# Optimization experiments

Hardware: AMD Instinct MI355X
Metric: run time of the kernel (lower is better)

## Reference

```python
import jax, jax.numpy as jnp
import numpy as np

P = 0.5          # dropout-style keep probability (wandb.config.probability)
Z = 1000         # number of Monte-Carlo normal draws in the original loop


def setup_inputs() -> dict:
    key = jax.random.key(0)
    k1, k2, k3 = jax.random.split(key, 3)
    B, D_in, H, C = 65536, 28 * 28, 256, 10
    x = jax.random.uniform(k1, (B, D_in), dtype=jnp.float32)          # pixel-like inputs in [0,1)
    W1 = jax.random.normal(k2, (H, D_in), dtype=jnp.float32) * 0.05   # fc1.weight
    W2 = jax.random.normal(k3, (C, H), dtype=jnp.float32) * 0.05      # fc2.weight
    return {"x": x, "W1": W1, "W2": W2}


def _mc_normal_layer(x, W, key):
    """Gaussian-dropout moment-propagation layer.

    Original torch code draws Z independent Normal(mean, std) samples and
    averages them, which is exactly Normal(mean, std / sqrt(Z)). We use the
    closed form: one eps draw instead of Z kernel launches.
    """
    mean = P * jnp.matmul(x, W.T)                                   # [B, out]
    var = P * (1.0 - P) * jnp.matmul(x * x, (W * W).T)              # [B, out]
    std = jnp.sqrt(var)
    eps = jax.random.normal(key, mean.shape, dtype=mean.dtype)
    return mean + std * (eps / jnp.sqrt(jnp.asarray(Z, mean.dtype)))


def reference(x, W1, W2):
    x = x.reshape(-1, 28 * 28)
    k1, k2 = jax.random.split(jax.random.key(42))
    h = jax.nn.relu(_mc_normal_layer(x, W1, k1))   # [B, H]
    out = _mc_normal_layer(h, W2, k2)              # [B, 10]
    return out
```

## Files before the change

### kernel.cpp

```cpp
#include <hip/hip_runtime.h>
#include <hip/hip_bf16.h>
#include <cstdint>


#define K_DIM 784
#define KP 800
#define N_HID 256
#define N_OUT 10
#define BM 64
#define NSTEP 25
#define WSQ_OFF (N_HID * KP)
#define W2_OFF (832 * 1024)
#define W2SQ 4096
#define H_OFF (1 << 20)
#define BM2 128

using short8 = __attribute__((ext_vector_type(8))) short;
using floatx4 = __attribute__((ext_vector_type(4))) float;
typedef uint16_t u16;

__host__ __device__ inline void threefry2x32(uint32_t k0, uint32_t k1,
                                             uint32_t x0, uint32_t x1,
                                             uint32_t& o0, uint32_t& o1) {
  uint32_t ks0 = k0, ks1 = k1, ks2 = k0 ^ k1 ^ 0x1BD11BDAu;
  x0 += ks0;
  x1 += ks1;
#define TFR(r) { x0 += x1; x1 = (x1 << (r)) | (x1 >> (32 - (r))); x1 ^= x0; }
  TFR(13) TFR(15) TFR(26) TFR(6)   x0 += ks1; x1 += ks2 + 1u;
  TFR(17) TFR(29) TFR(16) TFR(24)  x0 += ks2; x1 += ks0 + 2u;
  TFR(13) TFR(15) TFR(26) TFR(6)   x0 += ks0; x1 += ks1 + 3u;
  TFR(17) TFR(29) TFR(16) TFR(24)  x0 += ks1; x1 += ks2 + 4u;
  TFR(13) TFR(15) TFR(26) TFR(6)   x0 += ks2; x1 += ks0 + 5u;
#undef TFR
  o0 = x0;
  o1 = x1;
}

__device__ __forceinline__ float bits_to_normal(uint32_t bits) {
  const float lo = -0.99999994f;
  float u01 = __uint_as_float((bits >> 9) | 0x3F800000u) - 1.0f;
  float u = fmaxf(lo, u01 * 2.0f + lo);
  float w = -__logf((1.0f - u) * (1.0f + u));
  float p;
  if (w < 5.0f) {
    w -= 2.5f;
    p = 2.81022636e-08f;
    p = fmaf(p, w, 3.43273939e-07f);
    p = fmaf(p, w, -3.5233877e-06f);
    p = fmaf(p, w, -4.39150654e-06f);
    p = fmaf(p, w, 0.00021858087f);
    p = fmaf(p, w, -0.00125372503f);
    p = fmaf(p, w, -0.00417768164f);
    p = fmaf(p, w, 0.246640727f);
    p = fmaf(p, w, 1.50140941f);
  } else {
    w = sqrtf(w) - 3.0f;
    p = -0.000200214257f;
    p = fmaf(p, w, 0.000100950558f);
    p = fmaf(p, w, 0.00134934322f);
    p = fmaf(p, w, -0.00367342844f);
    p = fmaf(p, w, 0.00573950773f);
    p = fmaf(p, w, -0.0076224613f);
    p = fmaf(p, w, 0.00943887047f);
    p = fmaf(p, w, 1.00167406f);
    p = fmaf(p, w, 2.83297682f);
  }
  return 1.41421356f * (p * u);
}

__device__ __forceinline__ float eps_part(uint32_t ka, uint32_t kb, uint32_t i) {
  uint32_t o0, o1;
  threefry2x32(ka, kb, 0u, i, o0, o1);
  return bits_to_normal(o0 ^ o1);
}

__device__ __forceinline__ u16 cvt_bf16(float f) {
  union { __hip_bfloat16 h; u16 u; } c;
  c.h = __float2bfloat16(f);
  return c.u;
}

__device__ __forceinline__ float bf2f(u16 b) {
  return __uint_as_float((uint32_t)b << 16);
}

__global__ __launch_bounds__(256) void pack_w1(const float* __restrict__ W1,
                                               u16* __restrict__ bp) {
  const int col = blockIdx.x;
  for (int k = threadIdx.x; k < KP; k += 256) {
    float w = (k < K_DIM) ? W1[col * K_DIM + k] : 0.0f;
    bp[col * KP + k] = cvt_bf16(w);
    bp[WSQ_OFF + col * KP + k] = cvt_bf16(w * w);
  }
}

__global__ __launch_bounds__(256) void pack_w2(const float* __restrict__ W2,
                                               u16* __restrict__ w2p) {
#pragma unroll
  for (int i = 0; i < 16; ++i) {
    int g = threadIdx.x + i * 256;
    int col = g >> 8, k = g & 255;
    float w = (col < N_OUT) ? W2[col * N_HID + k] : 0.0f;
    w2p[g] = cvt_bf16(w);
    w2p[W2SQ + g] = cvt_bf16(w * w);
  }
}

__global__ __launch_bounds__(256, 4) void gemm1(
    const float* __restrict__ x, const u16* __restrict__ bp,
    u16* __restrict__ hws, uint32_t k1a, uint32_t k1b) {
  __shared__ u16 sA[2][2][BM * 32];

  const int tid = threadIdx.x;
  const int lane = tid & 63;
  const int l15 = lane & 15;
  const int lhal = lane >> 4;
  const int wn = tid >> 6;
  const int bid = blockIdx.x;
  const int gr0 = (bid >> 1) * BM;
  const int bc0 = (bid & 1) * 128;

  const int srow = tid >> 2;
  const int skq = (tid & 3) * 8;
  const float* xptr = x + (size_t)(gr0 + srow) * K_DIM + skq;
  const int sidx = (srow * 32 + skq) ^ ((srow & 7) << 3);

  const uint32_t boff0 = (uint32_t)(bc0 + wn * 32 + 0 * 16 + l15) * KP + (uint32_t)lhal * 8;
  const uint32_t boff1 = (uint32_t)(bc0 + wn * 32 + 1 * 16 + l15) * KP + (uint32_t)lhal * 8;

#define AIDX(i) ((((i * 16 + l15) * 32 + lhal * 8)) ^ (((i * 16 + l15) & 7) << 3))
  const int aidx0 = AIDX(0);
  const int aidx1 = AIDX(1);
  const int aidx2 = AIDX(2);
  const int aidx3 = AIDX(3);
#undef AIDX

#define DECL_ACC(i) \
  floatx4 am##i##0 = {0.f, 0.f, 0.f, 0.f}, am##i##1 = {0.f, 0.f, 0.f, 0.f}; \
  floatx4 av##i##0 = {0.f, 0.f, 0.f, 0.f}, av##i##1 = {0.f, 0.f, 0.f, 0.f};
  DECL_ACC(0) DECL_ACC(1) DECL_ACC(2) DECL_ACC(3)
#undef DECL_ACC

  float4 q0, q1;
  auto loadX = [&](int kk) {
    if (kk + skq + 8 <= K_DIM) {
      q0 = *reinterpret_cast<const float4*>(xptr + kk);
      q1 = *reinterpret_cast<const float4*>(xptr + kk + 4);
    } else {
      q0 = make_float4(0.f, 0.f, 0.f, 0.f);
      q1 = make_float4(0.f, 0.f, 0.f, 0.f);
    }
  };
  auto writeA = [&](int buf) {
    short8 va, v2;
    va[0] = (short)cvt_bf16(q0.x); v2[0] = (short)cvt_bf16(q0.x * q0.x);
    va[1] = (short)cvt_bf16(q0.y); v2[1] = (short)cvt_bf16(q0.y * q0.y);
    va[2] = (short)cvt_bf16(q0.z); v2[2] = (short)cvt_bf16(q0.z * q0.z);
    va[3] = (short)cvt_bf16(q0.w); v2[3] = (short)cvt_bf16(q0.w * q0.w);
    va[4] = (short)cvt_bf16(q1.x); v2[4] = (short)cvt_bf16(q1.x * q1.x);
    va[5] = (short)cvt_bf16(q1.y); v2[5] = (short)cvt_bf16(q1.y * q1.y);
    va[6] = (short)cvt_bf16(q1.z); v2[6] = (short)cvt_bf16(q1.z * q1.z);
    va[7] = (short)cvt_bf16(q1.w); v2[7] = (short)cvt_bf16(q1.w * q1.w);
    *reinterpret_cast<short8*>(&sA[buf][0][sidx]) = va;
    *reinterpret_cast<short8*>(&sA[buf][1][sidx]) = v2;
  };

  loadX(0);
  writeA(0);
  __syncthreads();

  for (int s = 0; s < NSTEP; ++s) {
    const int cur = s & 1, nxt = cur ^ 1;
    const bool have = (s + 1 < NSTEP);
    const int kk = s * 32;

    const u16* bpk = bp + kk;
    const short8 bm0 = *reinterpret_cast<const short8*>(&bpk[boff0]);
    const short8 bm1 = *reinterpret_cast<const short8*>(&bpk[boff1]);
    const short8 bv0 = *reinterpret_cast<const short8*>(&bpk[WSQ_OFF + boff0]);
    const short8 bv1 = *reinterpret_cast<const short8*>(&bpk[WSQ_OFF + boff1]);

    if (have) loadX(kk + 32);

    const u16* sc0 = &sA[cur][0][0];
    const u16* sc1 = &sA[cur][1][0];
#define STEP_I(i) { \
    const short8 af = *reinterpret_cast<const short8*>(&sc0[aidx##i]); \
    const short8 ag = *reinterpret_cast<const short8*>(&sc1[aidx##i]); \
    am##i##0 = __builtin_amdgcn_mfma_f32_16x16x32_bf16(af, bm0, am##i##0, 0, 0, 0); \
    av##i##0 = __builtin_amdgcn_mfma_f32_16x16x32_bf16(ag, bv0, av##i##0, 0, 0, 0); \
    am##i##1 = __builtin_amdgcn_mfma_f32_16x16x32_bf16(af, bm1, am##i##1, 0, 0, 0); \
    av##i##1 = __builtin_amdgcn_mfma_f32_16x16x32_bf16(ag, bv1, av##i##1, 0, 0, 0); }
    STEP_I(0) STEP_I(1) STEP_I(2) STEP_I(3)
#undef STEP_I

    if (have) writeA(nxt);
    __syncthreads();
  }

  const float INV = 0.031622776601683794f;
#define EPIG(AM, AV, G, I, J) do { \
    const int rl_ = I * 16 + lhal * 4 + (G); \
    const int c_ = bc0 + wn * 32 + J * 16 + l15; \
    float mean_ = 0.5f * (AM)[G]; \
    float sd_ = 0.5f * sqrtf((AV)[G]); \
    uint32_t idx_ = (uint32_t)(gr0 + rl_) * 256u + (uint32_t)c_; \
    float eps_ = eps_part(k1a, k1b, idx_); \
    float h_ = fmaxf(mean_ + sd_ * (eps_ * INV), 0.0f); \
    hws[(size_t)(gr0 + rl_) * 256 + c_] = cvt_bf16(h_); \
  } while (0)
#define EPI(i, j) do { \
    EPIG(am##i##j, av##i##j, 0, i, j); \
    EPIG(am##i##j, av##i##j, 1, i, j); \
    EPIG(am##i##j, av##i##j, 2, i, j); \
    EPIG(am##i##j, av##i##j, 3, i, j); \
  } while (0)
  EPI(0, 0); EPI(0, 1); EPI(1, 0); EPI(1, 1);
  EPI(2, 0); EPI(2, 1); EPI(3, 0); EPI(3, 1);
#undef EPI
#undef EPIG
}

__global__ __launch_bounds__(256, 4) void layer2(
    const u16* __restrict__ hws, const u16* __restrict__ w2p,
    float* __restrict__ out, uint32_t k2a, uint32_t k2b) {
  __shared__ u16 sH[2][BM2 * 32];

  const int tid = threadIdx.x;
  const int lane = tid & 63;
  const int l15 = lane & 15;
  const int lhal = lane >> 4;
  const int wv = tid >> 6;
  const int gr0 = blockIdx.x * BM2;

  const int srow = tid >> 1;
  const int sq = (tid & 1) * 16;
  const u16* hrow = hws + (size_t)(gr0 + srow) * 256 + sq;
  const int sidx0 = (srow * 32 + sq) ^ ((srow & 7) << 3);
  const int sidx1 = (srow * 32 + sq + 8) ^ ((srow & 7) << 3);

  const uint32_t boff = (uint32_t)l15 * 256 + (uint32_t)lhal * 8;

#define AIDX2(i) ((((wv * 32 + i * 16 + l15) * 32 + lhal * 8)) ^ (((wv * 32 + i * 16 + l15) & 7) << 3))
  const int aidx0 = AIDX2(0);
  const int aidx1 = AIDX2(1);
#undef AIDX2

  floatx4 am0 = {0.f, 0.f, 0.f, 0.f}, am1 = {0.f, 0.f, 0.f, 0.f};
  floatx4 av0 = {0.f, 0.f, 0.f, 0.f}, av1 = {0.f, 0.f, 0.f, 0.f};

  for (int s = 0; s < 8; ++s) {
    __syncthreads();
    const short8 c0 = *reinterpret_cast<const short8*>(&hrow[s * 32]);
    const short8 c1 = *reinterpret_cast<const short8*>(&hrow[s * 32 + 8]);
    short8 s0, s1;
#define SQE(D, S, E) { const float f_ = bf2f((u16)(S)[E]); (D)[E] = (short)cvt_bf16(f_ * f_); }
    SQE(s0, c0, 0) SQE(s0, c0, 1) SQE(s0, c0, 2) SQE(s0, c0, 3)
    SQE(s0, c0, 4) SQE(s0, c0, 5) SQE(s0, c0, 6) SQE(s0, c0, 7)
    SQE(s1, c1, 0) SQE(s1, c1, 1) SQE(s1, c1, 2) SQE(s1, c1, 3)
    SQE(s1, c1, 4) SQE(s1, c1, 5) SQE(s1, c1, 6) SQE(s1, c1, 7)
#undef SQE
    *reinterpret_cast<short8*>(&sH[0][sidx0]) = c0;
    *reinterpret_cast<short8*>(&sH[0][sidx1]) = c1;
    *reinterpret_cast<short8*>(&sH[1][sidx0]) = s0;
    *reinterpret_cast<short8*>(&sH[1][sidx1]) = s1;
    __syncthreads();

    const short8 bm = *reinterpret_cast<const short8*>(&w2p[boff + s * 32]);
    const short8 bv = *reinterpret_cast<const short8*>(&w2p[W2SQ + boff + s * 32]);
    const short8 af0 = *reinterpret_cast<const short8*>(&sH[0][aidx0]);
    const short8 af1 = *reinterpret_cast<const short8*>(&sH[0][aidx1]);
    const short8 ag0 = *reinterpret_cast<const short8*>(&sH[1][aidx0]);
    const short8 ag1 = *reinterpret_cast<const short8*>(&sH[1][aidx1]);
    am0 = __builtin_amdgcn_mfma_f32_16x16x32_bf16(af0, bm, am0, 0, 0, 0);
    av0 = __builtin_amdgcn_mfma_f32_16x16x32_bf16(ag0, bv, av0, 0, 0, 0);
    am1 = __builtin_amdgcn_mfma_f32_16x16x32_bf16(af1, bm, am1, 0, 0, 0);
    av1 = __builtin_amdgcn_mfma_f32_16x16x32_bf16(ag1, bv, av1, 0, 0, 0);
  }

  const float INV = 0.031622776601683794f;
  if (l15 < N_OUT) {
#define L2E(I, G) do { \
    const int row_ = gr0 + wv * 32 + I * 16 + lhal * 4 + (G); \
    float mean_ = 0.5f * am##I[G]; \
    float sd_ = 0.5f * sqrtf(av##I[G]); \
    float eps_ = eps_part(k2a, k2b, (uint32_t)row_ * 10u + (uint32_t)l15); \
    out[(size_t)row_ * 10 + l15] = mean_ + sd_ * (eps_ * INV); \
  } while (0)
    L2E(0, 0); L2E(0, 1); L2E(0, 2); L2E(0, 3);
    L2E(1, 0); L2E(1, 1); L2E(1, 2); L2E(1, 3);
#undef L2E
  }
}

extern "C" void kernel_launch(void* const* d_in, const int* in_sizes, int n_in,
                              void* d_out, int out_size, void* d_ws, size_t ws_size,
                              hipStream_t stream) {
  const float* x = (const float*)d_in[0];
  const float* W1 = (const float*)d_in[1];
  const float* W2 = (const float*)d_in[2];
  float* outp = (float*)d_out;
  u16* bp = (u16*)d_ws;
  u16* w2p = (u16*)((char*)d_ws + W2_OFF);
  u16* hws = (u16*)((char*)d_ws + H_OFF);

  uint32_t k1a, k1b, k2a, k2b;
  threefry2x32(0u, 42u, 0u, 0u, k1a, k1b);
  threefry2x32(0u, 42u, 0u, 1u, k2a, k2b);

  pack_w1<<<256, 256, 0, stream>>>(W1, bp);
  pack_w2<<<1, 256, 0, stream>>>(W2, w2p);
  gemm1<<<(65536 / BM) * 2, 256, 0, stream>>>(x, bp, hws, k1a, k1b);
  layer2<<<65536 / BM2, 256, 0, stream>>>(hws, w2p, outp, k2a, k2b);
}
```

Before: 160.2 us.

## Fuse layer-1 GEMM and layer-2 into one kernel with LDS-resident hidden activations

Merges gemm1 and layer2 into a single 1024-thread kernel. Each block computes a 128-row tile across all 256 hidden columns, stores the bf16 hidden activations in shared memory, and runs the small second GEMM from there, using a split-K reduction across two wave groups. This removes the global write and re-read of the 65536x256 hidden tensor, one kernel launch, and the duplicated x loads from splitting columns across two blocks. In exchange, blocks are larger with more shared memory, which lowers occupancy, and each thread now issues narrower x loads.

```diff
diff --git a/kernel.cpp b/kernel.cpp
--- a/kernel.cpp
+++ b/kernel.cpp
@@ -7,15 +7,15 @@
 #define KP 800
 #define N_HID 256
 #define N_OUT 10
-#define BM 64
+#define BMF 128
 #define NSTEP 25
 #define WSQ_OFF (N_HID * KP)
 #define W2_OFF (832 * 1024)
 #define W2SQ 4096
-#define H_OFF (1 << 20)
-#define BM2 128
+#define HSTR 264
 
 using short8 = __attribute__((ext_vector_type(8))) short;
+using short4v = __attribute__((ext_vector_type(4))) short;
 using floatx4 = __attribute__((ext_vector_type(4))) float;
 typedef uint16_t u16;
 
@@ -106,29 +106,31 @@
   }
 }
 
-__global__ __launch_bounds__(256, 4) void gemm1(
+__global__ __launch_bounds__(1024, 4) void fused(
     const float* __restrict__ x, const u16* __restrict__ bp,
-    u16* __restrict__ hws, uint32_t k1a, uint32_t k1b) {
-  __shared__ u16 sA[2][2][BM * 32];
+    const u16* __restrict__ w2p, float* __restrict__ out,
+    uint32_t k1a, uint32_t k1b, uint32_t k2a, uint32_t k2b) {
+  __shared__ u16 sA[2][2][BMF * 32];
+  __shared__ u16 hbuf[BMF * HSTR];
 
   const int tid = threadIdx.x;
   const int lane = tid & 63;
   const int l15 = lane & 15;
   const int lhal = lane >> 4;
-  const int wn = tid >> 6;
-  const int bid = blockIdx.x;
-  const int gr0 = (bid >> 1) * BM;
-  const int bc0 = (bid & 1) * 128;
-
-  const int srow = tid >> 2;
-  const int skq = (tid & 3) * 8;
+  const int wid = tid >> 6;
+  const int wm = wid >> 3;
+  const int wn = wid & 7;
+  const int gr0 = blockIdx.x * BMF;
+
+  const int srow = tid >> 3;
+  const int skq = (tid & 7) * 4;
   const float* xptr = x + (size_t)(gr0 + srow) * K_DIM + skq;
   const int sidx = (srow * 32 + skq) ^ ((srow & 7) << 3);
 
-  const uint32_t boff0 = (uint32_t)(bc0 + wn * 32 + 0 * 16 + l15) * KP + (uint32_t)lhal * 8;
-  const uint32_t boff1 = (uint32_t)(bc0 + wn * 32 + 1 * 16 + l15) * KP + (uint32_t)lhal * 8;
-
-#define AIDX(i) ((((i * 16 + l15) * 32 + lhal * 8)) ^ (((i * 16 + l15) & 7) << 3))
+  const uint32_t boff0 = (uint32_t)(wn * 32 + l15) * KP + (uint32_t)lhal * 8;
+  const uint32_t boff1 = boff0 + 16u * KP;
+
+#define AIDX(i) ((((wm * 64 + i * 16 + l15) * 32 + lhal * 8)) ^ ((l15 & 7) << 3))
   const int aidx0 = AIDX(0);
   const int aidx1 = AIDX(1);
   const int aidx2 = AIDX(2);
@@ -141,28 +143,22 @@
   DECL_ACC(0) DECL_ACC(1) DECL_ACC(2) DECL_ACC(3)
 #undef DECL_ACC
 
-  float4 q0, q1;
+  float4 q;
   auto loadX = [&](int kk) {
-    if (kk + skq + 8 <= K_DIM) {
-      q0 = *reinterpret_cast<const float4*>(xptr + kk);
-      q1 = *reinterpret_cast<const float4*>(xptr + kk + 4);
+    if (kk + skq + 4 <= K_DIM) {
+      q = *reinterpret_cast<const float4*>(xptr + kk);
     } else {
-      q0 = make_float4(0.f, 0.f, 0.f, 0.f);
-      q1 = make_float4(0.f, 0.f, 0.f, 0.f);
+      q = make_float4(0.f, 0.f, 0.f, 0.f);
     }
   };
   auto writeA = [&](int buf) {
-    short8 va, v2;
-    va[0] = (short)cvt_bf16(q0.x); v2[0] = (short)cvt_bf16(q0.x * q0.x);
-    va[1] = (short)cvt_bf16(q0.y); v2[1] = (short)cvt_bf16(q0.y * q0.y);
-    va[2] = (short)cvt_bf16(q0.z); v2[2] = (short)cvt_bf16(q0.z * q0.z);
-    va[3] = (short)cvt_bf16(q0.w); v2[3] = (short)cvt_bf16(q0.w * q0.w);
-    va[4] = (short)cvt_bf16(q1.x); v2[4] = (short)cvt_bf16(q1.x * q1.x);
-    va[5] = (short)cvt_bf16(q1.y); v2[5] = (short)cvt_bf16(q1.y * q1.y);
-    va[6] = (short)cvt_bf16(q1.z); v2[6] = (short)cvt_bf16(q1.z * q1.z);
-    va[7] = (short)cvt_bf16(q1.w); v2[7] = (short)cvt_bf16(q1.w * q1.w);
-    *reinterpret_cast<short8*>(&sA[buf][0][sidx]) = va;
-    *reinterpret_cast<short8*>(&sA[buf][1][sidx]) = v2;
+    short4v va, v2;
+    va[0] = (short)cvt_bf16(q.x); v2[0] = (short)cvt_bf16(q.x * q.x);
+    va[1] = (short)cvt_bf16(q.y); v2[1] = (short)cvt_bf16(q.y * q.y);
+    va[2] = (short)cvt_bf16(q.z); v2[2] = (short)cvt_bf16(q.z * q.z);
+    va[3] = (short)cvt_bf16(q.w); v2[3] = (short)cvt_bf16(q.w * q.w);
+    *reinterpret_cast<short4v*>(&sA[buf][0][sidx]) = va;
+    *reinterpret_cast<short4v*>(&sA[buf][1][sidx]) = v2;
   };
 
   loadX(0);
@@ -200,14 +196,14 @@
 
   const float INV = 0.031622776601683794f;
 #define EPIG(AM, AV, G, I, J) do { \
-    const int rl_ = I * 16 + lhal * 4 + (G); \
-    const int c_ = bc0 + wn * 32 + J * 16 + l15; \
+    const int rl_ = wm * 64 + I * 16 + lhal * 4 + (G); \
+    const int c_ = wn * 32 + J * 16 + l15; \
     float mean_ = 0.5f * (AM)[G]; \
     float sd_ = 0.5f * sqrtf((AV)[G]); \
     uint32_t idx_ = (uint32_t)(gr0 + rl_) * 256u + (uint32_t)c_; \
     float eps_ = eps_part(k1a, k1b, idx_); \
     float h_ = fmaxf(mean_ + sd_ * (eps_ * INV), 0.0f); \
-    hws[(size_t)(gr0 + rl_) * 256 + c_] = cvt_bf16(h_); \
+    hbuf[rl_ * HSTR + c_] = cvt_bf16(h_); \
   } while (0)
 #define EPI(i, j) do { \
     EPIG(am##i##j, av##i##j, 0, i, j); \
@@ -219,77 +215,64 @@
   EPI(2, 0); EPI(2, 1); EPI(3, 0); EPI(3, 1);
 #undef EPI
 #undef EPIG
-}
-
-__global__ __launch_bounds__(256, 4) void layer2(
-    const u16* __restrict__ hws, const u16* __restrict__ w2p,
-    float* __restrict__ out, uint32_t k2a, uint32_t k2b) {
-  __shared__ u16 sH[2][BM2 * 32];
-
-  const int tid = threadIdx.x;
-  const int lane = tid & 63;
-  const int l15 = lane & 15;
-  const int lhal = lane >> 4;
-  const int wv = tid >> 6;
-  const int gr0 = blockIdx.x * BM2;
-
-  const int srow = tid >> 1;
-  const int sq = (tid & 1) * 16;
-  const u16* hrow = hws + (size_t)(gr0 + srow) * 256 + sq;
-  const int sidx0 = (srow * 32 + sq) ^ ((srow & 7) << 3);
-  const int sidx1 = (srow * 32 + sq + 8) ^ ((srow & 7) << 3);
-
-  const uint32_t boff = (uint32_t)l15 * 256 + (uint32_t)lhal * 8;
-
-#define AIDX2(i) ((((wv * 32 + i * 16 + l15) * 32 + lhal * 8)) ^ (((wv * 32 + i * 16 + l15) & 7) << 3))
-  const int aidx0 = AIDX2(0);
-  const int aidx1 = AIDX2(1);
-#undef AIDX2
-
-  floatx4 am0 = {0.f, 0.f, 0.f, 0.f}, am1 = {0.f, 0.f, 0.f, 0.f};
-  floatx4 av0 = {0.f, 0.f, 0.f, 0.f}, av1 = {0.f, 0.f, 0.f, 0.f};
-
-  for (int s = 0; s < 8; ++s) {
-    __syncthreads();
-    const short8 c0 = *reinterpret_cast<const short8*>(&hrow[s * 32]);
-    const short8 c1 = *reinterpret_cast<const short8*>(&hrow[s * 32 + 8]);
-    short8 s0, s1;
-#define SQE(D, S, E) { const float f_ = bf2f((u16)(S)[E]); (D)[E] = (short)cvt_bf16(f_ * f_); }
-    SQE(s0, c0, 0) SQE(s0, c0, 1) SQE(s0, c0, 2) SQE(s0, c0, 3)
-    SQE(s0, c0, 4) SQE(s0, c0, 5) SQE(s0, c0, 6) SQE(s0, c0, 7)
-    SQE(s1, c1, 0) SQE(s1, c1, 1) SQE(s1, c1, 2) SQE(s1, c1, 3)
-    SQE(s1, c1, 4) SQE(s1, c1, 5) SQE(s1, c1, 6) SQE(s1, c1, 7)
-#undef SQE
-    *reinterpret_cast<short8*>(&sH[0][sidx0]) = c0;
-    *reinterpret_cast<short8*>(&sH[0][sidx1]) = c1;
-    *reinterpret_cast<short8*>(&sH[1][sidx0]) = s0;
-    *reinterpret_cast<short8*>(&sH[1][sidx1]) = s1;
-    __syncthreads();
-
-    const short8 bm = *reinterpret_cast<const short8*>(&w2p[boff + s * 32]);
-    const short8 bv = *reinterpret_cast<const short8*>(&w2p[W2SQ + boff + s * 32]);
-    const short8 af0 = *reinterpret_cast<const short8*>(&sH[0][aidx0]);
-    const short8 af1 = *reinterpret_cast<const short8*>(&sH[0][aidx1]);
-    const short8 ag0 = *reinterpret_cast<const short8*>(&sH[1][aidx0]);
-    const short8 ag1 = *reinterpret_cast<const short8*>(&sH[1][aidx1]);
-    am0 = __builtin_amdgcn_mfma_f32_16x16x32_bf16(af0, bm, am0, 0, 0, 0);
-    av0 = __builtin_amdgcn_mfma_f32_16x16x32_bf16(ag0, bv, av0, 0, 0, 0);
-    am1 = __builtin_amdgcn_mfma_f32_16x16x32_bf16(af1, bm, am1, 0, 0, 0);
-    av1 = __builtin_amdgcn_mfma_f32_16x16x32_bf16(ag1, bv, av1, 0, 0, 0);
-  }
-
-  const float INV = 0.031622776601683794f;
-  if (l15 < N_OUT) {
-#define L2E(I, G) do { \
-    const int row_ = gr0 + wv * 32 + I * 16 + lhal * 4 + (G); \
-    float mean_ = 0.5f * am##I[G]; \
-    float sd_ = 0.5f * sqrtf(av##I[G]); \
-    float eps_ = eps_part(k2a, k2b, (uint32_t)row_ * 10u + (uint32_t)l15); \
-    out[(size_t)row_ * 10 + l15] = mean_ + sd_ * (eps_ * INV); \
-  } while (0)
-    L2E(0, 0); L2E(0, 1); L2E(0, 2); L2E(0, 3);
-    L2E(1, 0); L2E(1, 1); L2E(1, 2); L2E(1, 3);
+  __syncthreads();
+
+  const int wq = wid & 7;
+  const int kh = wid >> 3;
+  const int kbase = kh * 128;
+  const int arow = wq * 16 + l15;
+  const uint32_t b2off = (uint32_t)l15 * 256 + (uint32_t)lhal * 8;
+  floatx4 am2 = {0.f, 0.f, 0.f, 0.f}, av2 = {0.f, 0.f, 0.f, 0.f};
+#define SQ8(DST, SRC) do { \
+    float f0_ = bf2f((u16)(SRC)[0]); (DST)[0] = (short)cvt_bf16(f0_ * f0_); \
+    float f1_ = bf2f((u16)(SRC)[1]); (DST)[1] = (short)cvt_bf16(f1_ * f1_); \
+    float f2_ = bf2f((u16)(SRC)[2]); (DST)[2] = (short)cvt_bf16(f2_ * f2_); \
+    float f3_ = bf2f((u16)(SRC)[3]); (DST)[3] = (short)cvt_bf16(f3_ * f3_); \
+    float f4_ = bf2f((u16)(SRC)[4]); (DST)[4] = (short)cvt_bf16(f4_ * f4_); \
+    float f5_ = bf2f((u16)(SRC)[5]); (DST)[5] = (short)cvt_bf16(f5_ * f5_); \
+    float f6_ = bf2f((u16)(SRC)[6]); (DST)[6] = (short)cvt_bf16(f6_ * f6_); \
+    float f7_ = bf2f((u16)(SRC)[7]); (DST)[7] = (short)cvt_bf16(f7_ * f7_); \
+  } while (0)
+#define L2S(T) do { \
+    const int k_ = kbase + (T) * 32; \
+    const short8 af_ = *reinterpret_cast<const short8*>(&hbuf[arow * HSTR + k_ + lhal * 8]); \
+    short8 ag_; \
+    SQ8(ag_, af_); \
+    const short8 bm_ = *reinterpret_cast<const short8*>(&w2p[b2off + k_]); \
+    const short8 bv_ = *reinterpret_cast<const short8*>(&w2p[W2SQ + b2off + k_]); \
+    am2 = __builtin_amdgcn_mfma_f32_16x16x32_bf16(af_, bm_, am2, 0, 0, 0); \
+    av2 = __builtin_amdgcn_mfma_f32_16x16x32_bf16(ag_, bv_, av2, 0, 0, 0); \
+  } while (0)
+  L2S(0); L2S(1); L2S(2); L2S(3);
+#undef L2S
+#undef SQ8
+
+  float* red = reinterpret_cast<float*>(&sA[0][0][0]);
+  if (kh == 1) {
+    const int rb = wq * 512 + lhal * 64 + l15;
+    red[rb + 0] = am2[0];  red[rb + 16] = am2[1];
+    red[rb + 32] = am2[2]; red[rb + 48] = am2[3];
+    red[rb + 256 + 0] = av2[0];  red[rb + 256 + 16] = av2[1];
+    red[rb + 256 + 32] = av2[2]; red[rb + 256 + 48] = av2[3];
+  }
+  __syncthreads();
+  if (kh == 0) {
+    const int rb = wq * 512 + lhal * 64 + l15;
+    am2[0] += red[rb + 0];  am2[1] += red[rb + 16];
+    am2[2] += red[rb + 32]; am2[3] += red[rb + 48];
+    av2[0] += red[rb + 256 + 0];  av2[1] += red[rb + 256 + 16];
+    av2[2] += red[rb + 256 + 32]; av2[3] += red[rb + 256 + 48];
+    if (l15 < N_OUT) {
+#define L2E(G) do { \
+      const int row_ = gr0 + wq * 16 + lhal * 4 + (G); \
+      float mean_ = 0.5f * am2[G]; \
+      float sd_ = 0.5f * sqrtf(av2[G]); \
+      float eps_ = eps_part(k2a, k2b, (uint32_t)row_ * 10u + (uint32_t)l15); \
+      out[(size_t)row_ * 10 + l15] = mean_ + sd_ * (eps_ * INV); \
+    } while (0)
+      L2E(0); L2E(1); L2E(2); L2E(3);
 #undef L2E
+    }
   }
 }
 
@@ -302,7 +285,6 @@
   float* outp = (float*)d_out;
   u16* bp = (u16*)d_ws;
   u16* w2p = (u16*)((char*)d_ws + W2_OFF);
-  u16* hws = (u16*)((char*)d_ws + H_OFF);
 
   uint32_t k1a, k1b, k2a, k2b;
   threefry2x32(0u, 42u, 0u, 0u, k1a, k1b);
@@ -310,6 +292,5 @@
 
   pack_w1<<<256, 256, 0, stream>>>(W1, bp);
   pack_w2<<<1, 256, 0, stream>>>(W2, w2p);
-  gemm1<<<(65536 / BM) * 2, 256, 0, stream>>>(x, bp, hws, k1a, k1b);
-  layer2<<<65536 / BM2, 256, 0, stream>>>(hws, w2p, outp, k2a, k2b);
-}
+  fused<<<65536 / BMF, 1024, 0, stream>>>(x, bp, w2p, outp, k1a, k1b, k2a, k2b);
+}
```

Measured after the change: 176.3 us. 1.1x slower.

## Load x fragments directly from global into MFMA registers, dropping LDS staging

Applied to the files above, without the earlier changes.

gemm1 no longer stages the bf16-converted x tile and its square through double-buffered shared memory. Each wave now reads its MFMA A fragments straight from global memory, converts and squares them in registers, and skips the per-step barrier. Every one of the four waves re-reads and re-converts the same x rows, so conversion work grows fourfold and more load traffic goes to L1/L2. The layer2 swizzle rewrite is equivalent because row offsets are multiples of 16.

```diff
diff --git a/kernel.cpp b/kernel.cpp
--- a/kernel.cpp
+++ b/kernel.cpp
@@ -7,7 +7,6 @@
 #define KP 800
 #define N_HID 256
 #define N_OUT 10
-#define BM 64
 #define NSTEP 25
 #define WSQ_OFF (N_HID * KP)
 #define W2_OFF (832 * 1024)
@@ -109,31 +108,22 @@
 __global__ __launch_bounds__(256, 4) void gemm1(
     const float* __restrict__ x, const u16* __restrict__ bp,
     u16* __restrict__ hws, uint32_t k1a, uint32_t k1b) {
-  __shared__ u16 sA[2][2][BM * 32];
-
   const int tid = threadIdx.x;
   const int lane = tid & 63;
   const int l15 = lane & 15;
   const int lhal = lane >> 4;
   const int wn = tid >> 6;
   const int bid = blockIdx.x;
-  const int gr0 = (bid >> 1) * BM;
+  const int gr0 = (bid >> 1) * 64;
   const int bc0 = (bid & 1) * 128;
 
-  const int srow = tid >> 2;
-  const int skq = (tid & 3) * 8;
-  const float* xptr = x + (size_t)(gr0 + srow) * K_DIM + skq;
-  const int sidx = (srow * 32 + skq) ^ ((srow & 7) << 3);
-
-  const uint32_t boff0 = (uint32_t)(bc0 + wn * 32 + 0 * 16 + l15) * KP + (uint32_t)lhal * 8;
-  const uint32_t boff1 = (uint32_t)(bc0 + wn * 32 + 1 * 16 + l15) * KP + (uint32_t)lhal * 8;
-
-#define AIDX(i) ((((i * 16 + l15) * 32 + lhal * 8)) ^ (((i * 16 + l15) & 7) << 3))
-  const int aidx0 = AIDX(0);
-  const int aidx1 = AIDX(1);
-  const int aidx2 = AIDX(2);
-  const int aidx3 = AIDX(3);
-#undef AIDX
+  const uint32_t boff0 = (uint32_t)(bc0 + wn * 32 + l15) * KP + (uint32_t)lhal * 8;
+  const uint32_t boff1 = boff0 + 16u * KP;
+
+  const float* ax0 = x + (size_t)(gr0 + l15) * K_DIM + lhal * 8;
+  const float* ax1 = ax0 + 16 * K_DIM;
+  const float* ax2 = ax0 + 32 * K_DIM;
+  const float* ax3 = ax0 + 48 * K_DIM;
 
 #define DECL_ACC(i) \
   floatx4 am##i##0 = {0.f, 0.f, 0.f, 0.f}, am##i##1 = {0.f, 0.f, 0.f, 0.f}; \
@@ -141,38 +131,9 @@
   DECL_ACC(0) DECL_ACC(1) DECL_ACC(2) DECL_ACC(3)
 #undef DECL_ACC
 
-  float4 q0, q1;
-  auto loadX = [&](int kk) {
-    if (kk + skq + 8 <= K_DIM) {
-      q0 = *reinterpret_cast<const float4*>(xptr + kk);
-      q1 = *reinterpret_cast<const float4*>(xptr + kk + 4);
-    } else {
-      q0 = make_float4(0.f, 0.f, 0.f, 0.f);
-      q1 = make_float4(0.f, 0.f, 0.f, 0.f);
-    }
-  };
-  auto writeA = [&](int buf) {
-    short8 va, v2;
-    va[0] = (short)cvt_bf16(q0.x); v2[0] = (short)cvt_bf16(q0.x * q0.x);
-    va[1] = (short)cvt_bf16(q0.y); v2[1] = (short)cvt_bf16(q0.y * q0.y);
-    va[2] = (short)cvt_bf16(q0.z); v2[2] = (short)cvt_bf16(q0.z * q0.z);
-    va[3] = (short)cvt_bf16(q0.w); v2[3] = (short)cvt_bf16(q0.w * q0.w);
-    va[4] = (short)cvt_bf16(q1.x); v2[4] = (short)cvt_bf16(q1.x * q1.x);
-    va[5] = (short)cvt_bf16(q1.y); v2[5] = (short)cvt_bf16(q1.y * q1.y);
-    va[6] = (short)cvt_bf16(q1.z); v2[6] = (short)cvt_bf16(q1.z * q1.z);
-    va[7] = (short)cvt_bf16(q1.w); v2[7] = (short)cvt_bf16(q1.w * q1.w);
-    *reinterpret_cast<short8*>(&sA[buf][0][sidx]) = va;
-    *reinterpret_cast<short8*>(&sA[buf][1][sidx]) = v2;
-  };
-
-  loadX(0);
-  writeA(0);
-  __syncthreads();
-
   for (int s = 0; s < NSTEP; ++s) {
-    const int cur = s & 1, nxt = cur ^ 1;
-    const bool have = (s + 1 < NSTEP);
     const int kk = s * 32;
+    const bool ok = (kk + lhal * 8) < K_DIM;
 
     const u16* bpk = bp + kk;
     const short8 bm0 = *reinterpret_cast<const short8*>(&bpk[boff0]);
@@ -180,22 +141,30 @@
     const short8 bv0 = *reinterpret_cast<const short8*>(&bpk[WSQ_OFF + boff0]);
     const short8 bv1 = *reinterpret_cast<const short8*>(&bpk[WSQ_OFF + boff1]);
 
-    if (have) loadX(kk + 32);
-
-    const u16* sc0 = &sA[cur][0][0];
-    const u16* sc1 = &sA[cur][1][0];
-#define STEP_I(i) { \
-    const short8 af = *reinterpret_cast<const short8*>(&sc0[aidx##i]); \
-    const short8 ag = *reinterpret_cast<const short8*>(&sc1[aidx##i]); \
-    am##i##0 = __builtin_amdgcn_mfma_f32_16x16x32_bf16(af, bm0, am##i##0, 0, 0, 0); \
-    av##i##0 = __builtin_amdgcn_mfma_f32_16x16x32_bf16(ag, bv0, av##i##0, 0, 0, 0); \
-    am##i##1 = __builtin_amdgcn_mfma_f32_16x16x32_bf16(af, bm1, am##i##1, 0, 0, 0); \
-    av##i##1 = __builtin_amdgcn_mfma_f32_16x16x32_bf16(ag, bv1, av##i##1, 0, 0, 0); }
-    STEP_I(0) STEP_I(1) STEP_I(2) STEP_I(3)
-#undef STEP_I
-
-    if (have) writeA(nxt);
-    __syncthreads();
+#define FRAG(i) { \
+    float4 p0_, p1_; \
+    if (ok) { \
+      p0_ = *reinterpret_cast<const float4*>(ax##i + kk); \
+      p1_ = *reinterpret_cast<const float4*>(ax##i + kk + 4); \
+    } else { \
+      p0_ = make_float4(0.f, 0.f, 0.f, 0.f); \
+      p1_ = make_float4(0.f, 0.f, 0.f, 0.f); \
+    } \
+    short8 af_, ag_; \
+    af_[0] = (short)cvt_bf16(p0_.x); ag_[0] = (short)cvt_bf16(p0_.x * p0_.x); \
+    af_[1] = (short)cvt_bf16(p0_.y); ag_[1] = (short)cvt_bf16(p0_.y * p0_.y); \
+    af_[2] = (short)cvt_bf16(p0_.z); ag_[2] = (short)cvt_bf16(p0_.z * p0_.z); \
+    af_[3] = (short)cvt_bf16(p0_.w); ag_[3] = (short)cvt_bf16(p0_.w * p0_.w); \
+    af_[4] = (short)cvt_bf16(p1_.x); ag_[4] = (short)cvt_bf16(p1_.x * p1_.x); \
+    af_[5] = (short)cvt_bf16(p1_.y); ag_[5] = (short)cvt_bf16(p1_.y * p1_.y); \
+    af_[6] = (short)cvt_bf16(p1_.z); ag_[6] = (short)cvt_bf16(p1_.z * p1_.z); \
+    af_[7] = (short)cvt_bf16(p1_.w); ag_[7] = (short)cvt_bf16(p1_.w * p1_.w); \
+    am##i##0 = __builtin_amdgcn_mfma_f32_16x16x32_bf16(af_, bm0, am##i##0, 0, 0, 0); \
+    av##i##0 = __builtin_amdgcn_mfma_f32_16x16x32_bf16(ag_, bv0, av##i##0, 0, 0, 0); \
+    am##i##1 = __builtin_amdgcn_mfma_f32_16x16x32_bf16(af_, bm1, am##i##1, 0, 0, 0); \
+    av##i##1 = __builtin_amdgcn_mfma_f32_16x16x32_bf16(ag_, bv1, av##i##1, 0, 0, 0); }
+    FRAG(0) FRAG(1) FRAG(2) FRAG(3)
+#undef FRAG
   }
 
   const float INV = 0.031622776601683794f;
@@ -241,7 +210,7 @@
 
   const uint32_t boff = (uint32_t)l15 * 256 + (uint32_t)lhal * 8;
 
-#define AIDX2(i) ((((wv * 32 + i * 16 + l15) * 32 + lhal * 8)) ^ (((wv * 32 + i * 16 + l15) & 7) << 3))
+#define AIDX2(i) ((((wv * 32 + i * 16 + l15) * 32 + lhal * 8)) ^ ((l15 & 7) << 3))
   const int aidx0 = AIDX2(0);
   const int aidx1 = AIDX2(1);
 #undef AIDX2
@@ -310,6 +279,6 @@
 
   pack_w1<<<256, 256, 0, stream>>>(W1, bp);
   pack_w2<<<1, 256, 0, stream>>>(W2, w2p);
-  gemm1<<<(65536 / BM) * 2, 256, 0, stream>>>(x, bp, hws, k1a, k1b);
+  gemm1<<<2048, 256, 0, stream>>>(x, bp, hws, k1a, k1b);
   layer2<<<65536 / BM2, 256, 0, stream>>>(hws, w2p, outp, k2a, k2b);
 }
```

Result: slower. 236.6 us (+47.7%).
